# Kernel tuning notes

Hardware: AMD Instinct MI355X
Metric: run time of the kernel (lower is better)

## Reference

```python
import jax, jax.numpy as jnp
import numpy as np
from jax import lax

N_STATES = 512
VOCAB = 32000
BATCH = 16
SEQ_LEN = 128


def setup_inputs() -> dict:
    key = jax.random.key(0)
    k_ids, k_em, k_tm, k_p = jax.random.split(key, 4)
    input_ids = jax.random.randint(k_ids, (BATCH, SEQ_LEN), 0, VOCAB, dtype=jnp.int64)
    em = jax.random.normal(k_em, (N_STATES, VOCAB), dtype=jnp.float32)
    tm = jax.random.normal(k_tm, (N_STATES, N_STATES), dtype=jnp.float32)
    p = jax.random.normal(k_p, (N_STATES,), dtype=jnp.float32)
    return {"input_ids": input_ids, "em": em, "tm": tm, "p": p}


def reference(input_ids, em, tm, p):
    """HMM forward algorithm in log space; returns mean NLL (scalar).

    em: [S, V] emission logits, tm: [S, S] transition logits, p: [S] prior logits.
    do_log_softmax=True -> normalize each in log space first.
    """
    log_em = jax.nn.log_softmax(em, axis=-1)   # [S, V]
    log_tm = jax.nn.log_softmax(tm, axis=-1)   # [S, S] rows = source state
    log_p = jax.nn.log_softmax(p, axis=-1)     # [S]

    # Gather emission log-probs per token: [B, T, S]
    em_tok = log_em.T[input_ids]

    # alpha_0[b, s] = log_p[s] + log_em[s, x_0]
    alpha0 = log_p[None, :] + em_tok[:, 0]     # [B, S]

    def step(alpha, e_t):
        # alpha: [B, S_src]; log-matmul: logsumexp over source states
        a = jax.nn.logsumexp(alpha[:, :, None] + log_tm[None, :, :], axis=1) + e_t
        return a, None

    em_rest = jnp.swapaxes(em_tok[:, 1:], 0, 1)  # [T-1, B, S]
    alpha_T, _ = lax.scan(step, alpha0, em_rest)

    # loss = -mean_b log p(x_b) = -mean_b logsumexp_s alpha_T[b, s]
    loss = -jnp.mean(jax.nn.logsumexp(alpha_T, axis=-1))
    return loss
```

## Files before the change

### kernel.cpp

```cpp
#include <hip/hip_runtime.h>
#include <hip/hip_bf16.h>

#define NS 512
#define NV 32000
#define NB 16
#define NT 128

#ifndef __has_builtin
#define __has_builtin(x) 0
#endif

typedef int v8i __attribute__((ext_vector_type(8)));
typedef float v4f __attribute__((ext_vector_type(4)));

__device__ inline unsigned enc_e4m3(float x) {
    x = fminf(x, 448.0f);
    unsigned u = __float_as_uint(x);
    if (x < 0.015625f) {
        return (unsigned)(int)rintf(x * 512.0f);
    }
    unsigned u2 = u + 0x7FFFFu + ((u >> 20) & 1u);
    return (((u2 >> 23) - 120u) << 3) | ((u2 >> 20) & 7u);
}

__device__ inline unsigned pack4_e4m3(float a, float b, float c, float d) {
#if __has_builtin(__builtin_amdgcn_cvt_pk_fp8_f32)
    int v = __builtin_amdgcn_cvt_pk_fp8_f32(a, b, 0, false);
    v = __builtin_amdgcn_cvt_pk_fp8_f32(c, d, v, true);
    return (unsigned)v;
#else
    return enc_e4m3(a) | (enc_e4m3(b) << 8) | (enc_e4m3(c) << 16) | (enc_e4m3(d) << 24);
#endif
}

#define DPPMAX(x, ctrl) \
    x = fmaxf(x, __int_as_float(__builtin_amdgcn_mov_dpp(__float_as_int(x), ctrl, 0xF, 0xF, true)))
#define DPPADD(x, ctrl) \
    x = x + __int_as_float(__builtin_amdgcn_mov_dpp(__float_as_int(x), ctrl, 0xF, 0xF, true))

#define UMX(a, b) ((a) > (b) ? (a) : (b))

__global__ __launch_bounds__(256) void k_emtok_T(
    const float* __restrict__ em, const int* __restrict__ ids,
    float* __restrict__ em_lin_T)
{
    const int s   = blockIdx.x;
    const int tid = threadIdx.x;
    const float* row = em + (size_t)s * NV;

    int idv[8];
#pragma unroll
    for (int k = 0; k < 8; ++k) idv[k] = ids[tid + 256 * k];
    float g[8];
#pragma unroll
    for (int k = 0; k < 8; ++k) g[k] = row[idv[k]];

    float sum = 0.f;
    const float4* row4 = (const float4*)row;
#pragma unroll 4
    for (int i = 0; i < 31; ++i) {
        float4 v = row4[tid + 256 * i];
        sum += __expf(v.x) + __expf(v.y) + __expf(v.z) + __expf(v.w);
    }
    sum += __expf(row[31744 + tid]);

#pragma unroll
    for (int off = 32; off; off >>= 1) sum += __shfl_down(sum, off);
    __shared__ float red[4];
    __shared__ float s_scale;
    if ((tid & 63) == 0) red[tid >> 6] = sum;
    __syncthreads();
    if (tid == 0) s_scale = (1.0f / ((red[0] + red[1]) + (red[2] + red[3]))) * 0x1p-18f;
    __syncthreads();
    const float scale = s_scale;

#pragma unroll
    for (int k = 0; k < 8; ++k)
        em_lin_T[(size_t)s * (NB * NT) + tid + 256 * k] = __expf(g[k]) * scale;
}

__global__ __launch_bounds__(256) void k_tr(
    const float* __restrict__ emT, float* __restrict__ em_lin)
{
    __shared__ float tile[32][33];
    const int jb = blockIdx.x * 32;
    const int sb = blockIdx.y * 32;
    const int cc = threadIdx.x & 31;
    const int rr = threadIdx.x >> 5;
#pragma unroll
    for (int i = 0; i < 4; ++i) {
        int r = rr + 8 * i;
        tile[r][cc] = emT[(size_t)(sb + r) * (NB * NT) + jb + cc];
    }
    __syncthreads();
#pragma unroll
    for (int i = 0; i < 4; ++i) {
        int r = rr + 8 * i;
        em_lin[(size_t)(jb + r) * NS + sb + cc] = tile[cc][r];
    }
}

__global__ __launch_bounds__(64) void k_z(
    const float* __restrict__ tm, float* __restrict__ zscale)
{
    const int k    = blockIdx.x;
    const int lane = threadIdx.x;
    const float* row = tm + (size_t)k * NS;

    float4 a = ((const float4*)row)[lane * 2];
    float4 b = ((const float4*)row)[lane * 2 + 1];
    float sum = ((__expf(a.x) + __expf(a.y)) + (__expf(a.z) + __expf(a.w)))
              + ((__expf(b.x) + __expf(b.y)) + (__expf(b.z) + __expf(b.w)));
#pragma unroll
    for (int off = 32; off; off >>= 1) sum += __shfl_down(sum, off);
    if (lane == 0) zscale[k] = 1024.0f / sum;
}

__global__ __launch_bounds__(256) void k_pt2(
    const float* __restrict__ tm, const float* __restrict__ zscale,
    unsigned char* __restrict__ PT)
{
    __shared__ float tile[64][65];
    __shared__ float zs[64];
    const int kb  = blockIdx.x * 64;
    const int db  = blockIdx.y * 64;
    const int tid = threadIdx.x;
    const int c   = tid & 63;
    const int r0  = tid >> 6;

    if (tid < 64) zs[tid] = zscale[kb + tid];
#pragma unroll
    for (int i = 0; i < 16; ++i) {
        int r = r0 + 4 * i;
        tile[r][c] = tm[(size_t)(kb + r) * NS + db + c];
    }
    __syncthreads();

    const int d  = tid >> 2;
    const int ks = (tid & 3) * 16;
    unsigned px[4];
#pragma unroll
    for (int gq = 0; gq < 4; ++gq) {
        int k0 = ks + gq * 4;
        px[gq] = pack4_e4m3(__expf(tile[k0 + 0][d]) * zs[k0 + 0],
                            __expf(tile[k0 + 1][d]) * zs[k0 + 1],
                            __expf(tile[k0 + 2][d]) * zs[k0 + 2],
                            __expf(tile[k0 + 3][d]) * zs[k0 + 3]);
    }
    uint4 o; o.x = px[0]; o.y = px[1]; o.z = px[2]; o.w = px[3];
    *(uint4*)(PT + (size_t)(db + d) * NS + kb + ks) = o;
}

__global__ __launch_bounds__(512, 2) void k_scan(
    const float* __restrict__ em_lin, const unsigned char* __restrict__ PT,
    const float* __restrict__ p, float* __restrict__ out)
{
    const int bb  = blockIdx.x;
    const int tid = threadIdx.x;
    const int w   = tid >> 6;
    const int l   = tid & 63;
    const int lc  = l & 15;
    const int lq  = l >> 4;

    __shared__ unsigned Ew[2][16 * 128];
    __shared__ __align__(16) unsigned char wmE[2][32];
    __shared__ float    wm2[8][4];
    __shared__ float    sbuf[4];

    v8i B[4][4];
#pragma unroll
    for (int nt = 0; nt < 4; ++nt) {
#pragma unroll
        for (int kt = 0; kt < 4; ++kt) {
            const uint4* src = (const uint4*)(PT + (size_t)((w * 4 + nt) * 16 + lc) * NS + kt * 128 + lq * 32);
            uint4 lo = src[0], hi = src[1];
            v8i bb8;
            bb8[0] = (int)lo.x; bb8[1] = (int)lo.y; bb8[2] = (int)lo.z; bb8[3] = (int)lo.w;
            bb8[4] = (int)hi.x; bb8[5] = (int)hi.y; bb8[6] = (int)hi.z; bb8[7] = (int)hi.w;
            B[nt][kt] = bb8;
        }
    }

    float zp = 0.f;
#pragma unroll
    for (int i = 0; i < 8; ++i) zp += __expf(p[l * 8 + i]);
    DPPADD(zp, 0x128); DPPADD(zp, 0x124); DPPADD(zp, 0xB1); DPPADD(zp, 0x4E);
    float Zp = __int_as_float(__builtin_amdgcn_readlane(__float_as_int(zp), 0))
             + __int_as_float(__builtin_amdgcn_readlane(__float_as_int(zp), 16))
             + __int_as_float(__builtin_amdgcn_readlane(__float_as_int(zp), 32))
             + __int_as_float(__builtin_amdgcn_readlane(__float_as_int(zp), 48));
    const float invZp = 1.0f / Zp;

    const int dbase0 = w * 64 + lc;
    const int gb     = bb * 4 + lq;

    const float* epb0 = em_lin + (size_t)gb * (NT * NS) + dbase0;
    float alpha[4];
#pragma unroll
    for (int nt = 0; nt < 4; ++nt)
        alpha[nt] = __expf(p[dbase0 + 16 * nt]) * invZp * epb0[16 * nt];

    int gsum = 18;
    const unsigned sel1 = (l & 1) ? 0x07030501u : 0x02060004u;
    const unsigned sel2 = (l & 2) ? 0x07060302u : 0x01000504u;
    const int mrow = 4 * lq + (l & 3);

    int aidx[8];
#pragma unroll
    for (int kt = 0; kt < 4; ++kt) {
#pragma unroll
        for (int c = 0; c < 2; ++c)
            aidx[kt * 2 + c] = lc * 32 + (((kt * 8 + lq * 2 + c) ^ lc) & 31);
    }
    int widx[4];
#pragma unroll
    for (int nt = 0; nt < 4; ++nt)
        widx[nt] = mrow * 128 + ((((w * 4 + nt) ^ mrow) & 31) << 2) + (lc >> 2);

    const int bA = lc >> 2;
    const int h  = lq >> 1;
    const unsigned shA = (unsigned)(bA << 3);
    const unsigned shQ = (unsigned)(lq << 3);

    const float* epb = epb0 + NS;

    for (int t = 1; t < NT; ++t) {
        const int buf = t & 1;
        unsigned* EwB = &Ew[buf][0];

        float epf[4];
#pragma unroll
        for (int nt = 0; nt < 4; ++nt) epf[nt] = epb[16 * nt];
        epb += NS;

        float mx = fmaxf(fmaxf(alpha[0], alpha[1]), fmaxf(alpha[2], alpha[3]));
        DPPMAX(mx, 0x128); DPPMAX(mx, 0x124); DPPMAX(mx, 0xB1); DPPMAX(mx, 0x4E);
        unsigned E = __float_as_uint(mx) >> 23;
        E = E > 1u ? E : 1u;
        const float sc = __uint_as_float((261u - E) << 23);

#pragma unroll
        for (int nt = 0; nt < 4; ++nt) {
            unsigned dw = pack4_e4m3(alpha[nt] * sc, 0.f, 0.f, 0.f);
            int tmp = __builtin_amdgcn_mov_dpp((int)dw, 0xB1, 0xF, 0xF, true);
            dw = __builtin_amdgcn_perm(dw, (unsigned)tmp, sel1);
            tmp = __builtin_amdgcn_mov_dpp((int)dw, 0x4E, 0xF, 0xF, true);
            dw = __builtin_amdgcn_perm(dw, (unsigned)tmp, sel2);
            EwB[widx[nt]] = dw;
        }
        if (lc == 0) wmE[buf][w * 4 + lq] = (unsigned char)E;
        __syncthreads();

        const uint4 ua = *(const uint4*)&wmE[buf][0];
        const uint4 ub = *(const uint4*)&wmE[buf][16];
        const unsigned d0 = ua.x, d1 = ua.y, d2 = ua.z, d3 = ua.w;
        const unsigned d4 = ub.x, d5 = ub.y, d6 = ub.z, d7 = ub.w;

        const unsigned a0 = (d0 >> shA) & 255u, a1 = (d1 >> shA) & 255u;
        const unsigned a2 = (d2 >> shA) & 255u, a3 = (d3 >> shA) & 255u;
        const unsigned a4 = (d4 >> shA) & 255u, a5 = (d5 >> shA) & 255u;
        const unsigned a6 = (d6 >> shA) & 255u, a7 = (d7 >> shA) & 255u;
        const unsigned MA = UMX(UMX(UMX(a0, a1), UMX(a2, a3)),
                                UMX(UMX(a4, a5), UMX(a6, a7)));

        const unsigned q0 = (d0 >> shQ) & 255u, q1 = (d1 >> shQ) & 255u;
        const unsigned q2 = (d2 >> shQ) & 255u, q3 = (d3 >> shQ) & 255u;
        const unsigned q4 = (d4 >> shQ) & 255u, q5 = (d5 >> shQ) & 255u;
        const unsigned q6 = (d6 >> shQ) & 255u, q7 = (d7 >> shQ) & 255u;
        const unsigned MQ = UMX(UMX(UMX(q0, q1), UMX(q2, q3)),
                                UMX(UMX(q4, q5), UMX(q6, q7)));
        gsum += (int)MQ - 126;

        const unsigned e0 = h ? a1 : a0;
        const unsigned e1 = h ? a3 : a2;
        const unsigned e2 = h ? a5 : a4;
        const unsigned e3 = h ? a7 : a6;
        int s0 = (int)e0 + 127 - (int)MA; s0 = s0 < 0 ? 0 : s0;
        int s1 = (int)e1 + 127 - (int)MA; s1 = s1 < 0 ? 0 : s1;
        int s2 = (int)e2 + 127 - (int)MA; s2 = s2 < 0 ? 0 : s2;
        int s3 = (int)e3 + 127 - (int)MA; s3 = s3 < 0 ? 0 : s3;
        const int scA[4] = { s0 * 0x01010101, s1 * 0x01010101,
                             s2 * 0x01010101, s3 * 0x01010101 };

        v8i A[4];
        const uint4* eb4 = (const uint4*)EwB;
#pragma unroll
        for (int kt = 0; kt < 4; ++kt) {
            uint4 lo = eb4[aidx[kt * 2 + 0]];
            uint4 hi = eb4[aidx[kt * 2 + 1]];
            v8i aa;
            aa[0] = (int)lo.x; aa[1] = (int)lo.y; aa[2] = (int)lo.z; aa[3] = (int)lo.w;
            aa[4] = (int)hi.x; aa[5] = (int)hi.y; aa[6] = (int)hi.z; aa[7] = (int)hi.w;
            A[kt] = aa;
        }

        v4f C[4];
#pragma unroll
        for (int nt = 0; nt < 4; ++nt) { C[nt][0] = 0.f; C[nt][1] = 0.f; C[nt][2] = 0.f; C[nt][3] = 0.f; }
#pragma unroll
        for (int kt = 0; kt < 4; ++kt)
#pragma unroll
            for (int nt = 0; nt < 4; ++nt)
                C[nt] = __builtin_amdgcn_mfma_scale_f32_16x16x128_f8f6f4(
                            A[kt], B[nt][kt], C[nt], 0, 0, 0, scA[kt], 0, 0x7F7F7F7F);

#pragma unroll
        for (int nt = 0; nt < 4; ++nt)
            alpha[nt] = C[nt][0] * epf[nt];
    }

    {
        float sm = (alpha[0] + alpha[1]) + (alpha[2] + alpha[3]);
        DPPADD(sm, 0x128); DPPADD(sm, 0x124); DPPADD(sm, 0xB1); DPPADD(sm, 0x4E);
        if (lc == 0) wm2[w][lq] = sm;
        if (w == 0 && lc == 0) sbuf[lq] = (float)gsum;
    }
    __syncthreads();
    if (tid < 4) {
        float s8 = ((wm2[0][tid] + wm2[1][tid]) + (wm2[2][tid] + wm2[3][tid]))
                 + ((wm2[4][tid] + wm2[5][tid]) + (wm2[6][tid] + wm2[7][tid]));
        float L2 = __log2f(s8) + sbuf[tid];
        atomicAdd(out, -(0.693147180559945f / 16.0f) * L2);
    }
}

extern "C" void kernel_launch(void* const* d_in, const int* in_sizes, int n_in,
                              void* d_out, int out_size, void* d_ws, size_t ws_size,
                              hipStream_t stream)
{
    const int*   ids = (const int*)d_in[0];
    const float* em  = (const float*)d_in[1];
    const float* tm  = (const float*)d_in[2];
    const float* p   = (const float*)d_in[3];
    float* out = (float*)d_out;

    float*          em_lin = (float*)d_ws;
    unsigned char*  PT     = (unsigned char*)d_ws + ((size_t)4 << 20);
    float*          zscale = (float*)((unsigned char*)d_ws + ((size_t)4 << 20) + ((size_t)256 << 10));
    float*          emT    = (float*)((unsigned char*)d_ws + ((size_t)4 << 20) + ((size_t)512 << 10));

    hipMemsetAsync(d_out, 0, sizeof(float), stream);

    k_emtok_T<<<NS, 256, 0, stream>>>(em, ids, emT);
    k_tr<<<dim3(64, 16), 256, 0, stream>>>(emT, em_lin);
    k_z<<<NS, 64, 0, stream>>>(tm, zscale);
    k_pt2<<<dim3(8, 8), 256, 0, stream>>>(tm, zscale, PT);
    k_scan<<<4, 512, 0, stream>>>(em_lin, PT, p, out);
}
```

Before: 244.5 us.

## Precompute block-wide exponent max one step ahead and vectorize emission loads

Four threads now compute the per-batch maximum of the wave exponents into a double-buffered byte array. The other threads read one precomputed byte instead of each reducing eight dwords after the barrier, which shortens the serial work between the barrier and the MFMAs. The emission tensor is written in a permuted state order so each lane fetches its four emission values with a single vector load. Exponent layout is reorganised so each lane reads its four scales as one dword, and the first MFMA starts from a zero constant. The scale is now also clamped at 254. The cross-iteration buffer handoff relies on the next step's barrier for ordering, which adds a subtle correctness dependency.

```diff
diff --git a/kernel.cpp b/kernel.cpp
--- a/kernel.cpp
+++ b/kernel.cpp
@@ -40,6 +40,14 @@
 
 #define UMX(a, b) ((a) > (b) ? (a) : (b))
 
+__device__ inline unsigned bytemax8(unsigned a, unsigned b) {
+    unsigned m0 = UMX(a & 255u, b & 255u);
+    unsigned m1 = UMX((a >> 8) & 255u, (b >> 8) & 255u);
+    unsigned m2 = UMX((a >> 16) & 255u, (b >> 16) & 255u);
+    unsigned m3 = UMX(a >> 24, b >> 24);
+    return UMX(UMX(m0, m1), UMX(m2, m3));
+}
+
 __global__ __launch_bounds__(256) void k_emtok_T(
     const float* __restrict__ em, const int* __restrict__ ids,
     float* __restrict__ em_lin_T)
@@ -96,7 +104,9 @@
 #pragma unroll
     for (int i = 0; i < 4; ++i) {
         int r = rr + 8 * i;
-        em_lin[(size_t)(jb + r) * NS + sb + cc] = tile[cc][r];
+        int s = sb + cc;
+        int ps = (s & ~63) | ((s & 15) << 2) | ((s >> 4) & 3);
+        em_lin[(size_t)(jb + r) * NS + ps] = tile[cc][r];
     }
 }
 
@@ -163,7 +173,8 @@
     const int lq  = l >> 4;
 
     __shared__ unsigned Ew[2][16 * 128];
-    __shared__ __align__(16) unsigned char wmE[2][32];
+    __shared__ __align__(4) unsigned char wmE2[2][32];
+    __shared__ __align__(4) unsigned char mbuf[2][4];
     __shared__ float    wm2[8][4];
     __shared__ float    sbuf[4];
 
@@ -173,10 +184,9 @@
 #pragma unroll
         for (int kt = 0; kt < 4; ++kt) {
             const uint4* src = (const uint4*)(PT + (size_t)((w * 4 + nt) * 16 + lc) * NS + kt * 128 + lq * 32);
-            uint4 lo = src[0], hi = src[1];
             v8i bb8;
-            bb8[0] = (int)lo.x; bb8[1] = (int)lo.y; bb8[2] = (int)lo.z; bb8[3] = (int)lo.w;
-            bb8[4] = (int)hi.x; bb8[5] = (int)hi.y; bb8[6] = (int)hi.z; bb8[7] = (int)hi.w;
+            *(uint4*)&bb8       = src[0];
+            *((uint4*)&bb8 + 1) = src[1];
             B[nt][kt] = bb8;
         }
     }
@@ -194,11 +204,12 @@
     const int dbase0 = w * 64 + lc;
     const int gb     = bb * 4 + lq;
 
-    const float* epb0 = em_lin + (size_t)gb * (NT * NS) + dbase0;
+    const float* epb0 = em_lin + (size_t)gb * (NT * NS) + (w * 64 + lc * 4);
+    v4f e0 = *(const v4f*)epb0;
     float alpha[4];
 #pragma unroll
     for (int nt = 0; nt < 4; ++nt)
-        alpha[nt] = __expf(p[dbase0 + 16 * nt]) * invZp * epb0[16 * nt];
+        alpha[nt] = __expf(p[dbase0 + 16 * nt]) * invZp * e0[nt];
 
     int gsum = 18;
     const unsigned sel1 = (l & 1) ? 0x07030501u : 0x02060004u;
@@ -219,18 +230,34 @@
 
     const int bA = lc >> 2;
     const int h  = lq >> 1;
+    const int wexp_w = (w & 1) * 16 + lq * 4 + (w >> 1);
+    const int wexp_r = h * 16 + bA * 4;
     const unsigned shA = (unsigned)(bA << 3);
     const unsigned shQ = (unsigned)(lq << 3);
 
     const float* epb = epb0 + NS;
+
+    {
+        float mx = fmaxf(fmaxf(alpha[0], alpha[1]), fmaxf(alpha[2], alpha[3]));
+        DPPMAX(mx, 0x128); DPPMAX(mx, 0x124); DPPMAX(mx, 0xB1); DPPMAX(mx, 0x4E);
+        unsigned E = __float_as_uint(mx) >> 23;
+        E = E > 1u ? E : 1u;
+        if (lc == 0) wmE2[1][wexp_w] = (unsigned char)E;
+    }
+    __syncthreads();
+    if (tid < 4) {
+        const unsigned u0 = *(const unsigned*)&wmE2[1][tid * 4];
+        const unsigned u1 = *(const unsigned*)&wmE2[1][16 + tid * 4];
+        mbuf[1][tid] = (unsigned char)bytemax8(u0, u1);
+    }
+
+    const v4f CZ = {0.f, 0.f, 0.f, 0.f};
 
     for (int t = 1; t < NT; ++t) {
         const int buf = t & 1;
         unsigned* EwB = &Ew[buf][0];
 
-        float epf[4];
-#pragma unroll
-        for (int nt = 0; nt < 4; ++nt) epf[nt] = epb[16 * nt];
+        v4f epf = *(const v4f*)epb;
         epb += NS;
 
         float mx = fmaxf(fmaxf(alpha[0], alpha[1]), fmaxf(alpha[2], alpha[3]));
@@ -248,57 +275,46 @@
             dw = __builtin_amdgcn_perm(dw, (unsigned)tmp, sel2);
             EwB[widx[nt]] = dw;
         }
-        if (lc == 0) wmE[buf][w * 4 + lq] = (unsigned char)E;
+        if (lc == 0) wmE2[buf][wexp_w] = (unsigned char)E;
         __syncthreads();
 
-        const uint4 ua = *(const uint4*)&wmE[buf][0];
-        const uint4 ub = *(const uint4*)&wmE[buf][16];
-        const unsigned d0 = ua.x, d1 = ua.y, d2 = ua.z, d3 = ua.w;
-        const unsigned d4 = ub.x, d5 = ub.y, d6 = ub.z, d7 = ub.w;
-
-        const unsigned a0 = (d0 >> shA) & 255u, a1 = (d1 >> shA) & 255u;
-        const unsigned a2 = (d2 >> shA) & 255u, a3 = (d3 >> shA) & 255u;
-        const unsigned a4 = (d4 >> shA) & 255u, a5 = (d5 >> shA) & 255u;
-        const unsigned a6 = (d6 >> shA) & 255u, a7 = (d7 >> shA) & 255u;
-        const unsigned MA = UMX(UMX(UMX(a0, a1), UMX(a2, a3)),
-                                UMX(UMX(a4, a5), UMX(a6, a7)));
-
-        const unsigned q0 = (d0 >> shQ) & 255u, q1 = (d1 >> shQ) & 255u;
-        const unsigned q2 = (d2 >> shQ) & 255u, q3 = (d3 >> shQ) & 255u;
-        const unsigned q4 = (d4 >> shQ) & 255u, q5 = (d5 >> shQ) & 255u;
-        const unsigned q6 = (d6 >> shQ) & 255u, q7 = (d7 >> shQ) & 255u;
-        const unsigned MQ = UMX(UMX(UMX(q0, q1), UMX(q2, q3)),
-                                UMX(UMX(q4, q5), UMX(q6, q7)));
-        gsum += (int)MQ - 126;
-
-        const unsigned e0 = h ? a1 : a0;
-        const unsigned e1 = h ? a3 : a2;
-        const unsigned e2 = h ? a5 : a4;
-        const unsigned e3 = h ? a7 : a6;
-        int s0 = (int)e0 + 127 - (int)MA; s0 = s0 < 0 ? 0 : s0;
-        int s1 = (int)e1 + 127 - (int)MA; s1 = s1 < 0 ? 0 : s1;
-        int s2 = (int)e2 + 127 - (int)MA; s2 = s2 < 0 ? 0 : s2;
-        int s3 = (int)e3 + 127 - (int)MA; s3 = s3 < 0 ? 0 : s3;
+        v8i A[4];
+        const uint4* eb4 = (const uint4*)EwB;
+#pragma unroll
+        for (int kt = 0; kt < 4; ++kt) {
+            v8i aa;
+            *(uint4*)&aa       = eb4[aidx[kt * 2 + 0]];
+            *((uint4*)&aa + 1) = eb4[aidx[kt * 2 + 1]];
+            A[kt] = aa;
+        }
+
+        if (tid < 4) {
+            const unsigned u0 = *(const unsigned*)&wmE2[buf][tid * 4];
+            const unsigned u1 = *(const unsigned*)&wmE2[buf][16 + tid * 4];
+            mbuf[buf ^ 1][tid] = (unsigned char)bytemax8(u0, u1);
+        }
+
+        const unsigned mdw = *(const unsigned*)&mbuf[buf][0];
+        const int MhA = (int)((mdw >> shA) & 255u);
+        const int MhQ = (int)((mdw >> shQ) & 255u);
+        gsum += MhQ - 126;
+
+        const unsigned dwE = *(const unsigned*)&wmE2[buf][wexp_r];
+        const int base = 127 - MhA;
+        int s0 = (int)(dwE & 255u) + base;         s0 = s0 < 0 ? 0 : (s0 > 254 ? 254 : s0);
+        int s1 = (int)((dwE >> 8) & 255u) + base;  s1 = s1 < 0 ? 0 : (s1 > 254 ? 254 : s1);
+        int s2 = (int)((dwE >> 16) & 255u) + base; s2 = s2 < 0 ? 0 : (s2 > 254 ? 254 : s2);
+        int s3 = (int)(dwE >> 24) + base;          s3 = s3 < 0 ? 0 : (s3 > 254 ? 254 : s3);
         const int scA[4] = { s0 * 0x01010101, s1 * 0x01010101,
                              s2 * 0x01010101, s3 * 0x01010101 };
 
-        v8i A[4];
-        const uint4* eb4 = (const uint4*)EwB;
-#pragma unroll
-        for (int kt = 0; kt < 4; ++kt) {
-            uint4 lo = eb4[aidx[kt * 2 + 0]];
-            uint4 hi = eb4[aidx[kt * 2 + 1]];
-            v8i aa;
-            aa[0] = (int)lo.x; aa[1] = (int)lo.y; aa[2] = (int)lo.z; aa[3] = (int)lo.w;
-            aa[4] = (int)hi.x; aa[5] = (int)hi.y; aa[6] = (int)hi.z; aa[7] = (int)hi.w;
-            A[kt] = aa;
-        }
-
         v4f C[4];
 #pragma unroll
-        for (int nt = 0; nt < 4; ++nt) { C[nt][0] = 0.f; C[nt][1] = 0.f; C[nt][2] = 0.f; C[nt][3] = 0.f; }
-#pragma unroll
-        for (int kt = 0; kt < 4; ++kt)
+        for (int nt = 0; nt < 4; ++nt)
+            C[nt] = __builtin_amdgcn_mfma_scale_f32_16x16x128_f8f6f4(
+                        A[0], B[nt][0], CZ, 0, 0, 0, scA[0], 0, 0x7F7F7F7F);
+#pragma unroll
+        for (int kt = 1; kt < 4; ++kt)
 #pragma unroll
             for (int nt = 0; nt < 4; ++nt)
                 C[nt] = __builtin_amdgcn_mfma_scale_f32_16x16x128_f8f6f4(
```

Measured after the change: 244.6 us. Within noise of the previous version (+0.0%).
